# Performance work log

Hardware: AMD Instinct MI355X
Metric: run time of the kernel (lower is better)

## Reference

```python
import jax, jax.numpy as jnp
import numpy as np

B, H, W, DIM = 16, 64, 64, 512
GH, GW = 8, 8
NH = 16
HD = DIM // NH
POS = DIM // 16  # DynamicPosBias pos_dim = (dim//4)//4 = 32
EPS = 1e-5


def setup_inputs() -> dict:
    key = jax.random.key(0)
    ks = jax.random.split(key, 12)
    w = lambda k, s: jax.random.normal(k, s, jnp.float32) * 0.02
    f32 = jnp.float32
    return {
        "x": jax.random.normal(ks[0], (B, H * W, DIM), f32),
        "norm1_g": jnp.ones((DIM,), f32), "norm1_b": jnp.zeros((DIM,), f32),
        "qkv_w": w(ks[1], (3 * DIM, DIM)), "qkv_b": jnp.zeros((3 * DIM,), f32),
        "proj_w": w(ks[2], (DIM, DIM)), "proj_b": jnp.zeros((DIM,), f32),
        "pos_w0": w(ks[3], (POS, 2)), "pos_b0": jnp.zeros((POS,), f32),
        "pos_ln0_g": jnp.ones((POS,), f32), "pos_ln0_b": jnp.zeros((POS,), f32),
        "pos_w1": w(ks[4], (POS, POS)), "pos_b1": jnp.zeros((POS,), f32),
        "pos_ln1_g": jnp.ones((POS,), f32), "pos_ln1_b": jnp.zeros((POS,), f32),
        "pos_w2": w(ks[5], (POS, POS)), "pos_b2": jnp.zeros((POS,), f32),
        "pos_ln2_g": jnp.ones((POS,), f32), "pos_ln2_b": jnp.zeros((POS,), f32),
        "pos_w3": w(ks[6], (NH, POS)), "pos_b3": jnp.zeros((NH,), f32),
        "norm2_g": jnp.ones((DIM,), f32), "norm2_b": jnp.zeros((DIM,), f32),
        "mlp_w1": w(ks[7], (4 * DIM, DIM)), "mlp_b1": jnp.zeros((4 * DIM,), f32),
        "mlp_w2": w(ks[8], (DIM, 4 * DIM)), "mlp_b2": jnp.zeros((DIM,), f32),
    }


def _ln(x, g, b):
    m = jnp.mean(x, -1, keepdims=True)
    v = jnp.mean(jnp.square(x - m), -1, keepdims=True)
    return (x - m) * jax.lax.rsqrt(v + EPS) * g + b


def _rel_bias_tables():
    # relative coordinate table [(2GH-1)*(2GW-1), 2]
    ph = jnp.arange(1 - GH, GH)
    pw = jnp.arange(1 - GW, GW)
    biases = jnp.stack(jnp.meshgrid(ph, pw, indexing="ij")).reshape(2, -1).T.astype(jnp.float32)
    # relative position index [GH*GW, GH*GW]
    coords = jnp.stack(jnp.meshgrid(jnp.arange(GH), jnp.arange(GW), indexing="ij")).reshape(2, -1)
    rel = (coords[:, :, None] - coords[:, None, :]).transpose(1, 2, 0)  # [N,N,2]
    idx = (rel[..., 0] + GH - 1) * (2 * GW - 1) + (rel[..., 1] + GW - 1)
    return biases, idx


def reference(x, norm1_g, norm1_b, qkv_w, qkv_b, proj_w, proj_b,
              pos_w0, pos_b0, pos_ln0_g, pos_ln0_b,
              pos_w1, pos_b1, pos_ln1_g, pos_ln1_b,
              pos_w2, pos_b2, pos_ln2_g, pos_ln2_b,
              pos_w3, pos_b3, norm2_g, norm2_b,
              mlp_w1, mlp_b1, mlp_w2, mlp_b2):
    biases, rel_idx = _rel_bias_tables()
    Ng = GH * GW
    scale = HD ** -0.5

    shortcut = x
    h = _ln(x, norm1_g, norm1_b).reshape(B, H, W, DIM)
    # use_lda=True: long-distance (strided) grouping
    h = h.reshape(B, GH, H // GH, GW, W // GW, DIM).transpose(0, 2, 4, 1, 3, 5)
    h = h.reshape(B * (H * W) // Ng, Ng, DIM)  # [G, Ng, C]

    # attention
    qkv = h @ qkv_w.T + qkv_b
    qkv = qkv.reshape(-1, Ng, 3, NH, HD).transpose(2, 0, 3, 1, 4)  # [3,G,NH,Ng,HD]
    q, k, v = qkv[0], qkv[1], qkv[2]
    attn = jnp.einsum("ghnd,ghmd->ghnm", q * scale, k)

    # dynamic position bias MLP on the coordinate table
    p = jax.nn.relu(_ln(biases @ pos_w0.T + pos_b0, pos_ln0_g, pos_ln0_b))
    p = jax.nn.relu(_ln(p @ pos_w1.T + pos_b1, pos_ln1_g, pos_ln1_b))
    p = jax.nn.relu(_ln(p @ pos_w2.T + pos_b2, pos_ln2_g, pos_ln2_b))
    p = p @ pos_w3.T + pos_b3  # [(2GH-1)(2GW-1), NH]
    rel_bias = p[rel_idx].transpose(2, 0, 1)  # [NH, Ng, Ng]

    attn = jax.nn.softmax(attn + rel_bias[None], axis=-1)
    o = jnp.einsum("ghnm,ghmd->ghnd", attn, v)
    o = o.transpose(0, 2, 1, 3).reshape(-1, Ng, DIM)
    o = o @ proj_w.T + proj_b

    # ungroup (inverse of lda grouping)
    o = o.reshape(B, H // GH, W // GW, GH, GW, DIM)
    o = o.transpose(0, 3, 1, 4, 2, 5).reshape(B, H * W, DIM)

    x = shortcut + o
    m = _ln(x, norm2_g, norm2_b)
    m = jax.nn.gelu(m @ mlp_w1.T + mlp_b1, approximate=False)
    m = m @ mlp_w2.T + mlp_b2
    return x + m
```

## Files before the change

### kernel.cpp

```cpp
#include <hip/hip_runtime.h>
#include <hip/hip_bf16.h>

typedef __bf16 bf16;
typedef __bf16 bf16x8 __attribute__((ext_vector_type(8)));
typedef float f32x4_t __attribute__((ext_vector_type(4)));

static constexpr int kDIM = 512;

static constexpr size_t OFF_QKVW = 0;
static constexpr size_t OFF_PROJW = 1572864;
static constexpr size_t OFF_W1   = 2097152;
static constexpr size_t OFF_W2   = 4194304;
static constexpr size_t OFF_PTAB = 6291456;
static constexpr size_t OFF_A    = 8388608;
static constexpr size_t OFF_B    = 276824064;

typedef __attribute__((address_space(3))) uint32_t lds_u32_t;
typedef __attribute__((address_space(1))) const uint32_t glb_u32_t;
#define ASYNC_COPY16(gp, lp) __builtin_amdgcn_global_load_lds((glb_u32_t*)(gp), (lds_u32_t*)(lp), 16, 0, 0)
#define WAITV0() asm volatile("s_waitcnt vmcnt(0)" ::: "memory")

__global__ __launch_bounds__(256)
void cast_all_k(const float* __restrict__ qkvw, const float* __restrict__ pjw,
                const float* __restrict__ w1, const float* __restrict__ w2,
                unsigned char* __restrict__ qkvw8, unsigned char* __restrict__ pjw8,
                unsigned char* __restrict__ w18, unsigned char* __restrict__ w28)
{
    int i = blockIdx.x * blockDim.x + threadIdx.x;
    if (i < 196608) {
        float4 v = ((const float4*)qkvw)[i];
        int p = __builtin_amdgcn_cvt_pk_fp8_f32(v.x * 64.0f, v.y * 64.0f, 0, false);
        p = __builtin_amdgcn_cvt_pk_fp8_f32(v.z * 64.0f, v.w * 64.0f, p, true);
        ((unsigned int*)qkvw8)[i] = (unsigned int)p;
    } else if (i < 262144) {
        int ii = i - 196608;
        float4 v = ((const float4*)pjw)[ii];
        int idx = ii * 4;
        int row = idx >> 9;
        int j0 = idx & 511;
        float vv[4] = {v.x, v.y, v.z, v.w};
#pragma unroll
        for (int t = 0; t < 4; ++t) {
            int j = j0 + t;
            int pj = (j & ~31) | ((j & 7) << 2) | (((j >> 4) & 1) << 1) | ((j >> 3) & 1);
            int p8 = __builtin_amdgcn_cvt_pk_fp8_f32(vv[t] * 64.0f, vv[t] * 64.0f, 0, false);
            pjw8[(size_t)row * 512 + pj] = (unsigned char)(p8 & 0xff);
        }
    } else if (i < 524288) {
        int ii = i - 262144;
        float4 v = ((const float4*)w1)[ii];
        int p = __builtin_amdgcn_cvt_pk_fp8_f32(v.x * 64.0f, v.y * 64.0f, 0, false);
        p = __builtin_amdgcn_cvt_pk_fp8_f32(v.z * 64.0f, v.w * 64.0f, p, true);
        ((unsigned int*)w18)[ii] = (unsigned int)p;
    } else {
        int ii = i - 524288;
        float4 v = ((const float4*)w2)[ii];
        int idx = ii * 4;
        int row = idx >> 11;
        int j0 = idx & 2047;
        float vv[4] = {v.x, v.y, v.z, v.w};
#pragma unroll
        for (int t = 0; t < 4; ++t) {
            int j = j0 + t;
            int pj = (j & ~127) | (j & 64) | ((j & 15) << 2) | ((j >> 4) & 3);
            int p8 = __builtin_amdgcn_cvt_pk_fp8_f32(vv[t] * 64.0f, vv[t] * 64.0f, 0, false);
            w28[(size_t)row * 2048 + pj] = (unsigned char)(p8 & 0xff);
        }
    }
}

template<int GROUP>
__global__ __launch_bounds__(256)
void ln_k(const float* __restrict__ x, const float* __restrict__ gw,
          const float* __restrict__ bw, unsigned char* __restrict__ out)
{
    const int t = blockIdx.x * 4 + (threadIdx.x >> 6);
    const int lane = threadIdx.x & 63;
    const float* xp = x + (size_t)t * kDIM + lane * 8;
    float4 p0 = *(const float4*)xp;
    float4 p1 = *(const float4*)(xp + 4);
    float v[8] = {p0.x, p0.y, p0.z, p0.w, p1.x, p1.y, p1.z, p1.w};
    float s = 0.f;
#pragma unroll
    for (int i = 0; i < 8; ++i) s += v[i];
#pragma unroll
    for (int off = 32; off > 0; off >>= 1) s += __shfl_xor(s, off);
    const float mean = s * (1.0f / 512.0f);
    float q = 0.f;
#pragma unroll
    for (int i = 0; i < 8; ++i) { float d = v[i] - mean; q += d * d; }
#pragma unroll
    for (int off = 32; off > 0; off >>= 1) q += __shfl_xor(q, off);
    const float rstd = rsqrtf(q * (1.0f / 512.0f) + 1e-5f);
    size_t orow;
    if (GROUP) {
        int b = t >> 12, r = (t >> 6) & 63, c = t & 63;
        int g = b * 64 + (r & 7) * 8 + (c & 7);
        int n = (r >> 3) * 8 + (c >> 3);
        orow = (size_t)g * 64 + n;
    } else {
        orow = t;
    }
    float4 g0 = *(const float4*)(gw + lane * 8);
    float4 g1 = *(const float4*)(gw + lane * 8 + 4);
    float4 b0 = *(const float4*)(bw + lane * 8);
    float4 b1 = *(const float4*)(bw + lane * 8 + 4);
    float gg[8] = {g0.x, g0.y, g0.z, g0.w, g1.x, g1.y, g1.z, g1.w};
    float bb[8] = {b0.x, b0.y, b0.z, b0.w, b1.x, b1.y, b1.z, b1.w};
    float o[8];
#pragma unroll
    for (int i = 0; i < 8; ++i) o[i] = ((v[i] - mean) * rstd * gg[i] + bb[i]) * 32.0f;
    unsigned int lo = 0, hi = 0;
    lo = (unsigned int)__builtin_amdgcn_cvt_pk_fp8_f32(o[0], o[1], 0, false);
    lo = (unsigned int)__builtin_amdgcn_cvt_pk_fp8_f32(o[2], o[3], (int)lo, true);
    hi = (unsigned int)__builtin_amdgcn_cvt_pk_fp8_f32(o[4], o[5], 0, false);
    hi = (unsigned int)__builtin_amdgcn_cvt_pk_fp8_f32(o[6], o[7], (int)hi, true);
    uint2 u; u.x = lo; u.y = hi;
    *(uint2*)(out + orow * kDIM + lane * 8) = u;
}

__device__ inline void ln32_relu(float* h, const float* g, const float* b)
{
    float m = 0.f;
#pragma unroll
    for (int i = 0; i < 32; ++i) m += h[i];
    m *= (1.0f / 32.0f);
    float v = 0.f;
#pragma unroll
    for (int i = 0; i < 32; ++i) { float d = h[i] - m; v += d * d; }
    v *= (1.0f / 32.0f);
    float r = rsqrtf(v + 1e-5f);
#pragma unroll
    for (int i = 0; i < 32; ++i) h[i] = fmaxf((h[i] - m) * r * g[i] + b[i], 0.f);
}

__global__ __launch_bounds__(256)
void posmlp_k(const float* __restrict__ w0, const float* __restrict__ b0,
              const float* __restrict__ g0, const float* __restrict__ bb0,
              const float* __restrict__ w1, const float* __restrict__ b1,
              const float* __restrict__ g1, const float* __restrict__ bb1,
              const float* __restrict__ w2, const float* __restrict__ b2,
              const float* __restrict__ g2, const float* __restrict__ bb2,
              const float* __restrict__ w3, const float* __restrict__ b3,
              float* __restrict__ ptab)
{
    int r = threadIdx.x;
    if (r >= 225) return;
    float in0 = (float)(r / 15) - 7.0f;
    float in1 = (float)(r % 15) - 7.0f;
    float h[32], h2[32];
#pragma unroll
    for (int o = 0; o < 32; ++o) h[o] = w0[o * 2] * in0 + w0[o * 2 + 1] * in1 + b0[o];
    ln32_relu(h, g0, bb0);
#pragma unroll
    for (int o = 0; o < 32; ++o) {
        float s = b1[o];
#pragma unroll
        for (int i = 0; i < 32; ++i) s += w1[o * 32 + i] * h[i];
        h2[o] = s;
    }
    ln32_relu(h2, g1, bb1);
#pragma unroll
    for (int o = 0; o < 32; ++o) {
        float s = b2[o];
#pragma unroll
        for (int i = 0; i < 32; ++i) s += w2[o * 32 + i] * h2[i];
        h[o] = s;
    }
    ln32_relu(h, g2, bb2);
#pragma unroll
    for (int o = 0; o < 16; ++o) {
        float s = b3[o];
#pragma unroll
        for (int i = 0; i < 32; ++i) s += w3[o * 32 + i] * h[i];
        ptab[r * 16 + o] = s;
    }
}

__global__ __launch_bounds__(256)
void attn_mfma_k(const unsigned char* __restrict__ qkv, const float* __restrict__ ptab,
                 unsigned char* __restrict__ obuf)
{
    const int g  = blockIdx.x >> 1;
    const int hb = blockIdx.x & 1;
    const int w  = threadIdx.x >> 6;
    const int lane = threadIdx.x & 63;
    const int c = lane & 15, q = lane >> 4;

    __shared__ float ptl[16][240];
    __shared__ alignas(16) bf16 pl[4][4096];
    __shared__ alignas(16) bf16 vt[4][2048];

    for (int i = threadIdx.x; i < 3600; i += 256)
        ptl[i & 15][i >> 4] = ptab[i];
    __syncthreads();

    const size_t rowb = (size_t)g * 64;
    bf16* pw = pl[w];
    char* vw = (char*)vt[w];

    for (int hh = 0; hh < 2; ++hh) {
        const int head = hb * 8 + hh * 4 + w;
        const unsigned char* qb = qkv + rowb * 2048 + head * 32;

        const bf16* vbase = (const bf16*)(qb + 1024 + head * 32);
        bf16x8 vrow[4];
#pragma unroll
        for (int l = 0; l < 4; ++l)
            vrow[l] = *(const bf16x8*)((const bf16*)((const char*)vbase + (size_t)lane * 2048) + l * 8);

        long aq[4], bk[4];
#pragma unroll
        for (int i = 0; i < 4; ++i) {
            aq[i] = *(const long*)(qb + (size_t)(i * 16 + c) * 2048 + q * 8);
            bk[i] = *(const long*)(qb + 512 + (size_t)(i * 16 + c) * 2048 + q * 8);
        }

        f32x4_t s[4][4];
#pragma unroll
        for (int i = 0; i < 4; ++i)
#pragma unroll
            for (int j = 0; j < 4; ++j)
                s[i][j] = __builtin_amdgcn_mfma_f32_16x16x32_fp8_fp8(aq[i], bk[j],
                          (f32x4_t){0.f, 0.f, 0.f, 0.f}, 0, 0, 0);

#pragma unroll
        for (int l = 0; l < 4; ++l)
#pragma unroll
            for (int j = 0; j < 8; ++j) {
                const int d = l * 8 + j;
                *(bf16*)(vw + d * 128 + ((lane * 2) ^ ((d & 7) << 4))) = vrow[l][j];
            }

        const float scale = 0.17677669529663687f / 1024.0f;
        float inv[4][4];
#pragma unroll
        for (int i = 0; i < 4; ++i)
#pragma unroll
            for (int jj = 0; jj < 4; ++jj) {
                const int n = i * 16 + q * 4 + jj;
                const int na = n >> 3, nu = n & 7;
                float mx = -1e30f;
#pragma unroll
                for (int j = 0; j < 4; ++j) {
                    const int m = j * 16 + c;
                    const int idx = (na - (m >> 3) + 7) * 15 + (nu - (m & 7) + 7);
                    float v = s[i][j][jj] * scale + ptl[head][idx];
                    s[i][j][jj] = v;
                    mx = fmaxf(mx, v);
                }
#pragma unroll
                for (int off = 1; off < 16; off <<= 1) mx = fmaxf(mx, __shfl_xor(mx, off));
                float sum = 0.f;
#pragma unroll
                for (int j = 0; j < 4; ++j) {
                    float e = __expf(s[i][j][jj] - mx);
                    s[i][j][jj] = e; sum += e;
                }
#pragma unroll
                for (int off = 1; off < 16; off <<= 1) sum += __shfl_xor(sum, off);
                inv[i][jj] = __fdividef(1.0f, sum);
            }

#pragma unroll
        for (int i = 0; i < 4; ++i)
#pragma unroll
            for (int jj = 0; jj < 4; ++jj) {
                const int n = i * 16 + q * 4 + jj;
                const int swz = (n & 7) << 4;
#pragma unroll
                for (int j = 0; j < 4; ++j) {
                    const int m = j * 16 + c;
                    *(bf16*)((char*)pw + n * 128 + ((m * 2) ^ swz)) = (bf16)s[i][j][jj];
                }
            }

        bf16x8 bv[2][2];
#pragma unroll
        for (int ks = 0; ks < 2; ++ks)
#pragma unroll
            for (int dt = 0; dt < 2; ++dt)
                bv[ks][dt] = *(const bf16x8*)(vw + (dt * 16 + c) * 128 +
                              ((ks * 64 + q * 16) ^ ((c & 7) << 4)));

        f32x4_t o[4][2];
#pragma unroll
        for (int i = 0; i < 4; ++i)
#pragma unroll
            for (int dt = 0; dt < 2; ++dt)
                o[i][dt] = (f32x4_t){0.f, 0.f, 0.f, 0.f};
#pragma unroll
        for (int ks = 0; ks < 2; ++ks)
#pragma unroll
            for (int i = 0; i < 4; ++i) {
                const int n = i * 16 + c;
                bf16x8 ap = *(const bf16x8*)((char*)pw + n * 128 +
                             ((ks * 64 + q * 16) ^ ((n & 7) << 4)));
#pragma unroll
                for (int dt = 0; dt < 2; ++dt)
                    o[i][dt] = __builtin_amdgcn_mfma_f32_16x16x32_bf16(ap, bv[ks][dt], o[i][dt], 0, 0, 0);
            }

        unsigned char* ob = obuf + rowb * 512 + head * 32;
#pragma unroll
        for (int i = 0; i < 4; ++i)
#pragma unroll
            for (int jj = 0; jj < 4; ++jj) {
                const int n = i * 16 + q * 4 + jj;
                float v0 = o[i][0][jj] * inv[i][jj] * 32.0f;
                float v1 = o[i][1][jj] * inv[i][jj] * 32.0f;
                int p8 = __builtin_amdgcn_cvt_pk_fp8_f32(v0, v1, 0, false);
                *(unsigned short*)(ob + (size_t)n * 512 + c * 2) = (unsigned short)(p8 & 0xffff);
            }
    }
}

template<int MODE, int NBX, int K>
__global__ __launch_bounds__(256, 2)
void gemm_fp8(const unsigned char* __restrict__ A, const unsigned char* __restrict__ Bw,
              const float* __restrict__ bias, const float* __restrict__ resid,
              void* __restrict__ outp, int N, float invs)
{
    __shared__ alignas(16) unsigned char As[128 * 128];
    __shared__ alignas(16) unsigned char Bs[128 * 128];
    const int tid = threadIdx.x;
    const int lane = tid & 63;
    const int w = tid >> 6;
    const int wr = w >> 1, wc = w & 1;
    const int c = lane & 15, q = lane >> 4;

    const int bid = blockIdx.y * NBX + blockIdx.x;
    const int nwg = gridDim.y * NBX;
    const int swz = (bid & 7) * (nwg >> 3) + (bid >> 3);
    const int by = swz / NBX;
    const int bx = swz - by * NBX;
    const int rowBase = by * 128;
    const int colBase = bx * 128;

    f32x4_t acc[4][4];
#pragma unroll
    for (int m = 0; m < 4; ++m)
#pragma unroll
        for (int n = 0; n < 4; ++n)
            acc[m][n] = (f32x4_t){0.f, 0.f, 0.f, 0.f};

    const int key = c & 7;
    const int hb8 = (q & 1) * 8;

    const int sg = (tid & 7) ^ ((tid >> 3) & 7);
    const unsigned char* aBase = A + (size_t)(rowBase + (tid >> 3)) * K + sg * 16;
    const unsigned char* bBase = Bw + (size_t)(colBase + (tid >> 3)) * K + sg * 16;
    unsigned char* ldsA = As + (tid & 192) * 16;
    unsigned char* ldsB = Bs + (tid & 192) * 16;

#pragma unroll 2
    for (int kt = 0; kt < K; kt += 128) {
#pragma unroll
        for (int l = 0; l < 4; ++l) {
            ASYNC_COPY16(aBase + (size_t)l * 32 * K + kt, ldsA + l * 4096);
            ASYNC_COPY16(bBase + (size_t)l * 32 * K + kt, ldsB + l * 4096);
        }
        WAITV0();
        __syncthreads();
#pragma unroll
        for (int kk = 0; kk < 4; ++kk) {
            const int sb = (((2 * kk + (q >> 1)) ^ key) << 4) + hb8;
            long af[4], bfr[4];
#pragma unroll
            for (int m = 0; m < 4; ++m) {
                const int row = wr * 64 + m * 16 + c;
                af[m] = *(const long*)((const char*)As + row * 128 + sb);
            }
#pragma unroll
            for (int n = 0; n < 4; ++n) {
                const int row = wc * 64 + n * 16 + c;
                bfr[n] = *(const long*)((const char*)Bs + row * 128 + sb);
            }
#pragma unroll
            for (int m = 0; m < 4; ++m)
#pragma unroll
                for (int n = 0; n < 4; ++n)
                    acc[m][n] = __builtin_amdgcn_mfma_f32_16x16x32_fp8_fp8(af[m], bfr[n], acc[m][n], 0, 0, 0);
        }
        __syncthreads();
    }

#pragma unroll
    for (int m = 0; m < 4; ++m) {
#pragma unroll
        for (int jj = 0; jj < 4; ++jj) {
            int grow = rowBase + wr * 64 + m * 16 + q * 4 + jj;
            float vv[4];
#pragma unroll
            for (int n = 0; n < 4; ++n)
                vv[n] = acc[m][n][jj] * invs + bias[colBase + wc * 64 + n * 16 + c];
            if constexpr (MODE == 0) {
                char* ob = (char*)outp;
                if (colBase < 1024) {
                    int p0 = __builtin_amdgcn_cvt_pk_fp8_f32(vv[0] * 32.0f, vv[1] * 32.0f, 0, false);
                    int p1 = __builtin_amdgcn_cvt_pk_fp8_f32(vv[2] * 32.0f, vv[3] * 32.0f, 0, false);
                    *(unsigned short*)(ob + (size_t)grow * 2048 + colBase + wc * 64 + c * 2) =
                        (unsigned short)(p0 & 0xffff);
                    *(unsigned short*)(ob + (size_t)grow * 2048 + colBase + wc * 64 + 32 + c * 2) =
                        (unsigned short)(p1 & 0xffff);
                } else {
                    bf16 t0 = (bf16)vv[0], t1 = (bf16)vv[1], t2 = (bf16)vv[2], t3 = (bf16)vv[3];
                    unsigned int pk0 = ((unsigned int)*(unsigned short*)&t1 << 16) |
                                       (unsigned int)*(unsigned short*)&t0;
                    unsigned int pk1 = ((unsigned int)*(unsigned short*)&t3 << 16) |
                                       (unsigned int)*(unsigned short*)&t2;
                    size_t vb = (size_t)grow * 2048 + 1024 + (size_t)(colBase - 1024 + wc * 64) * 2;
                    *(unsigned int*)(ob + vb + c * 4) = pk0;
                    *(unsigned int*)(ob + vb + 64 + c * 4) = pk1;
                }
            } else if constexpr (MODE == 1) {
#pragma unroll
                for (int n = 0; n < 4; ++n) {
                    float v = vv[n];
                    float e = __expf(1.5957691216057308f * (v + 0.044715f * v * v * v));
                    vv[n] = v * __fdividef(e, 1.0f + e) * 64.0f;
                }
                int p = __builtin_amdgcn_cvt_pk_fp8_f32(vv[0], vv[1], 0, false);
                p = __builtin_amdgcn_cvt_pk_fp8_f32(vv[2], vv[3], p, true);
                *(unsigned int*)((char*)outp + (size_t)grow * N + colBase + wc * 64 + c * 4) =
                    (unsigned int)p;
            } else {
#pragma unroll
                for (int n = 0; n < 4; ++n) {
                    int gcol = colBase + wc * 64 + n * 16 + c;
                    float v = vv[n];
                    if constexpr (MODE == 2) {
                        int g = grow >> 6, ns = grow & 63;
                        int b = g >> 6, i = (g >> 3) & 7, j = g & 7;
                        int a = ns >> 3, u = ns & 7;
                        int t = b * 4096 + (a * 8 + i) * 64 + (u * 8 + j);
                        size_t oi = (size_t)t * 512 + gcol;
                        ((float*)outp)[oi] = resid[oi] + v;
                    } else {
                        size_t oi = (size_t)grow * 512 + gcol;
                        ((float*)outp)[oi] = resid[oi] + v;
                    }
                }
            }
        }
    }
}

extern "C" void kernel_launch(void* const* d_in, const int* in_sizes, int n_in,
                              void* d_out, int out_size, void* d_ws, size_t ws_size,
                              hipStream_t stream)
{
    const float* x    = (const float*)d_in[0];
    const float* n1g  = (const float*)d_in[1];
    const float* n1b  = (const float*)d_in[2];
    const float* qkvw = (const float*)d_in[3];
    const float* qkvb = (const float*)d_in[4];
    const float* pjw  = (const float*)d_in[5];
    const float* pjb  = (const float*)d_in[6];
    const float* pw0  = (const float*)d_in[7];
    const float* pb0  = (const float*)d_in[8];
    const float* pg0  = (const float*)d_in[9];
    const float* pbb0 = (const float*)d_in[10];
    const float* pw1  = (const float*)d_in[11];
    const float* pb1  = (const float*)d_in[12];
    const float* pg1  = (const float*)d_in[13];
    const float* pbb1 = (const float*)d_in[14];
    const float* pw2  = (const float*)d_in[15];
    const float* pb2  = (const float*)d_in[16];
    const float* pg2  = (const float*)d_in[17];
    const float* pbb2 = (const float*)d_in[18];
    const float* pw3  = (const float*)d_in[19];
    const float* pb3  = (const float*)d_in[20];
    const float* n2g  = (const float*)d_in[21];
    const float* n2b  = (const float*)d_in[22];
    const float* w1   = (const float*)d_in[23];
    const float* b1   = (const float*)d_in[24];
    const float* w2   = (const float*)d_in[25];
    const float* b2   = (const float*)d_in[26];

    char* ws = (char*)d_ws;
    unsigned char* qkvw_f8 = (unsigned char*)(ws + OFF_QKVW);
    unsigned char* pjw_f8  = (unsigned char*)(ws + OFF_PROJW);
    unsigned char* w1_f8 = (unsigned char*)(ws + OFF_W1);
    unsigned char* w2_f8 = (unsigned char*)(ws + OFF_W2);
    float* ptab  = (float*)(ws + OFF_PTAB);
    unsigned char* bufA8 = (unsigned char*)(ws + OFF_A);
    unsigned char* bufB8 = (unsigned char*)(ws + OFF_B);
    float* xout  = (float*)d_out;

    cast_all_k<<<3072, 256, 0, stream>>>(qkvw, pjw, w1, w2, qkvw_f8, pjw_f8, w1_f8, w2_f8);

    posmlp_k<<<1, 256, 0, stream>>>(pw0, pb0, pg0, pbb0, pw1, pb1, pg1, pbb1,
                                    pw2, pb2, pg2, pbb2, pw3, pb3, ptab);

    ln_k<1><<<16384, 256, 0, stream>>>(x, n1g, n1b, bufB8);

    gemm_fp8<0, 12, 512><<<dim3(12, 512), 256, 0, stream>>>(bufB8, qkvw_f8, qkvb, nullptr,
                                                            bufA8, 1536, 1.0f / 2048.0f);

    attn_mfma_k<<<2048, 256, 0, stream>>>(bufA8, ptab, bufB8);

    gemm_fp8<2, 4, 512><<<dim3(4, 512), 256, 0, stream>>>(bufB8, pjw_f8, pjb, x,
                                                          xout, 512, 1.0f / 2048.0f);

    ln_k<0><<<16384, 256, 0, stream>>>(xout, n2g, n2b, bufB8);

    gemm_fp8<1, 16, 512><<<dim3(16, 512), 256, 0, stream>>>(bufB8, w1_f8, b1, nullptr,
                                                            bufA8, 2048, 1.0f / 2048.0f);

    gemm_fp8<3, 4, 2048><<<dim3(4, 512), 256, 0, stream>>>(bufA8, w2_f8, b2, xout,
                                                           xout, 512, 1.0f / 4096.0f);
}
```

Before: 662.8 us.

## Use 32x32x16 FP8 MFMA GEMM kernel for MLP layers

Adds a new FP8 GEMM kernel built on 32x32x16 MFMA instructions with swizzled LDS tiles and an XOR-keyed layout, and uses it for the two MLP GEMMs. The W1 output layout (GELU epilogue writing fp8 pairs) and the W2 weight permutation are changed to match the new MFMA operand layout. The intent is higher MFMA throughput and fewer LDS reads per flop than the 16x16 variant. It risks register pressure, since launch bounds request 2 blocks per CU with four 16-wide accumulators, and it risks layout mismatches between the producer and consumer GEMMs.

```diff
diff --git a/kernel.cpp b/kernel.cpp
--- a/kernel.cpp
+++ b/kernel.cpp
@@ -4,6 +4,7 @@
 typedef __bf16 bf16;
 typedef __bf16 bf16x8 __attribute__((ext_vector_type(8)));
 typedef float f32x4_t __attribute__((ext_vector_type(4)));
+typedef float f32x16_t __attribute__((ext_vector_type(16)));
 
 static constexpr int kDIM = 512;
 
@@ -62,7 +63,7 @@
 #pragma unroll
         for (int t = 0; t < 4; ++t) {
             int j = j0 + t;
-            int pj = (j & ~127) | (j & 64) | ((j & 15) << 2) | ((j >> 4) & 3);
+            int pj = (j & ~63) | ((j & 31) << 1) | ((j >> 5) & 1);
             int p8 = __builtin_amdgcn_cvt_pk_fp8_f32(vv[t] * 64.0f, vv[t] * 64.0f, 0, false);
             w28[(size_t)row * 2048 + pj] = (unsigned char)(p8 & 0xff);
         }
@@ -413,34 +414,105 @@
                     *(unsigned int*)(ob + vb + c * 4) = pk0;
                     *(unsigned int*)(ob + vb + 64 + c * 4) = pk1;
                 }
-            } else if constexpr (MODE == 1) {
-#pragma unroll
-                for (int n = 0; n < 4; ++n) {
-                    float v = vv[n];
-                    float e = __expf(1.5957691216057308f * (v + 0.044715f * v * v * v));
-                    vv[n] = v * __fdividef(e, 1.0f + e) * 64.0f;
-                }
-                int p = __builtin_amdgcn_cvt_pk_fp8_f32(vv[0], vv[1], 0, false);
-                p = __builtin_amdgcn_cvt_pk_fp8_f32(vv[2], vv[3], p, true);
-                *(unsigned int*)((char*)outp + (size_t)grow * N + colBase + wc * 64 + c * 4) =
-                    (unsigned int)p;
             } else {
 #pragma unroll
                 for (int n = 0; n < 4; ++n) {
                     int gcol = colBase + wc * 64 + n * 16 + c;
                     float v = vv[n];
-                    if constexpr (MODE == 2) {
-                        int g = grow >> 6, ns = grow & 63;
-                        int b = g >> 6, i = (g >> 3) & 7, j = g & 7;
-                        int a = ns >> 3, u = ns & 7;
-                        int t = b * 4096 + (a * 8 + i) * 64 + (u * 8 + j);
-                        size_t oi = (size_t)t * 512 + gcol;
-                        ((float*)outp)[oi] = resid[oi] + v;
-                    } else {
-                        size_t oi = (size_t)grow * 512 + gcol;
-                        ((float*)outp)[oi] = resid[oi] + v;
-                    }
+                    int g = grow >> 6, ns = grow & 63;
+                    int b = g >> 6, i = (g >> 3) & 7, j = g & 7;
+                    int a = ns >> 3, u = ns & 7;
+                    int t = b * 4096 + (a * 8 + i) * 64 + (u * 8 + j);
+                    size_t oi = (size_t)t * 512 + gcol;
+                    ((float*)outp)[oi] = resid[oi] + v;
                 }
+            }
+        }
+    }
+}
+
+template<int MODE, int NBX, int K>
+__global__ __launch_bounds__(256, 2)
+void gemm_fp8_32(const unsigned char* __restrict__ A, const unsigned char* __restrict__ Bw,
+                 const float* __restrict__ bias, const float* __restrict__ resid,
+                 void* __restrict__ outp, int N, float invs)
+{
+    __shared__ alignas(16) unsigned char As[128 * 128];
+    __shared__ alignas(16) unsigned char Bs[128 * 128];
+    const int tid = threadIdx.x;
+    const int lane = tid & 63;
+    const int w = tid >> 6;
+    const int wr = w >> 1, wc = w & 1;
+    const int c32 = lane & 31, hb = lane >> 5;
+
+    const int bid = blockIdx.y * NBX + blockIdx.x;
+    const int nwg = gridDim.y * NBX;
+    const int swz = (bid & 7) * (nwg >> 3) + (bid >> 3);
+    const int by = swz / NBX;
+    const int bx = swz - by * NBX;
+    const int rowBase = by * 128;
+    const int colBase = bx * 128;
+
+    f32x16_t acc00 = {0.f,0.f,0.f,0.f,0.f,0.f,0.f,0.f,0.f,0.f,0.f,0.f,0.f,0.f,0.f,0.f};
+    f32x16_t acc01 = acc00, acc10 = acc00, acc11 = acc00;
+
+    const int key = c32 & 7;
+    const int hb8 = hb * 8;
+    const int rA0 = (wr * 64 + c32) * 128;
+    const int rB0 = (wc * 64 + c32) * 128;
+
+    const int sg = (tid & 7) ^ ((tid >> 3) & 7);
+    const unsigned char* aBase = A + (size_t)(rowBase + (tid >> 3)) * K + sg * 16;
+    const unsigned char* bBase = Bw + (size_t)(colBase + (tid >> 3)) * K + sg * 16;
+    unsigned char* ldsA = As + (tid & 192) * 16;
+    unsigned char* ldsB = Bs + (tid & 192) * 16;
+
+#pragma unroll 2
+    for (int kt = 0; kt < K; kt += 128) {
+#pragma unroll
+        for (int l = 0; l < 4; ++l) {
+            ASYNC_COPY16(aBase + (size_t)l * 32 * K + kt, ldsA + l * 4096);
+            ASYNC_COPY16(bBase + (size_t)l * 32 * K + kt, ldsB + l * 4096);
+        }
+        WAITV0();
+        __syncthreads();
+#pragma unroll
+        for (int ks = 0; ks < 8; ++ks) {
+            const int so = ((ks ^ key) << 4) + hb8;
+            long a0 = *(const long*)((const char*)As + rA0 + so);
+            long a1 = *(const long*)((const char*)As + rA0 + 32 * 128 + so);
+            long b0 = *(const long*)((const char*)Bs + rB0 + so);
+            long b1 = *(const long*)((const char*)Bs + rB0 + 32 * 128 + so);
+            acc00 = __builtin_amdgcn_mfma_f32_32x32x16_fp8_fp8(a0, b0, acc00, 0, 0, 0);
+            acc01 = __builtin_amdgcn_mfma_f32_32x32x16_fp8_fp8(a0, b1, acc01, 0, 0, 0);
+            acc10 = __builtin_amdgcn_mfma_f32_32x32x16_fp8_fp8(a1, b0, acc10, 0, 0, 0);
+            acc11 = __builtin_amdgcn_mfma_f32_32x32x16_fp8_fp8(a1, b1, acc11, 0, 0, 0);
+        }
+        __syncthreads();
+    }
+
+    const float bs0 = bias[colBase + wc * 64 + c32];
+    const float bs1 = bias[colBase + wc * 64 + 32 + c32];
+#pragma unroll
+    for (int mt = 0; mt < 2; ++mt) {
+#pragma unroll
+        for (int r = 0; r < 16; ++r) {
+            const int grow = rowBase + wr * 64 + mt * 32 + (r & 3) + ((r >> 2) << 3) + hb * 4;
+            float v0 = (mt == 0 ? acc00[r] : acc10[r]) * invs + bs0;
+            float v1 = (mt == 0 ? acc01[r] : acc11[r]) * invs + bs1;
+            if constexpr (MODE == 1) {
+                float e0 = __expf(1.5957691216057308f * (v0 + 0.044715f * v0 * v0 * v0));
+                v0 = v0 * __fdividef(e0, 1.0f + e0) * 64.0f;
+                float e1 = __expf(1.5957691216057308f * (v1 + 0.044715f * v1 * v1 * v1));
+                v1 = v1 * __fdividef(e1, 1.0f + e1) * 64.0f;
+                int p = __builtin_amdgcn_cvt_pk_fp8_f32(v0, v1, 0, false);
+                *(unsigned short*)((char*)outp + (size_t)grow * N + colBase + wc * 64 + c32 * 2) =
+                    (unsigned short)(p & 0xffff);
+            } else {
+                size_t o0 = (size_t)grow * 512 + colBase + wc * 64 + c32;
+                size_t o1 = o0 + 32;
+                ((float*)outp)[o0] = resid[o0] + v0;
+                ((float*)outp)[o1] = resid[o1] + v1;
             }
         }
     }
@@ -505,9 +577,9 @@
 
     ln_k<0><<<16384, 256, 0, stream>>>(xout, n2g, n2b, bufB8);
 
-    gemm_fp8<1, 16, 512><<<dim3(16, 512), 256, 0, stream>>>(bufB8, w1_f8, b1, nullptr,
-                                                            bufA8, 2048, 1.0f / 2048.0f);
-
-    gemm_fp8<3, 4, 2048><<<dim3(4, 512), 256, 0, stream>>>(bufA8, w2_f8, b2, xout,
-                                                           xout, 512, 1.0f / 4096.0f);
-}
+    gemm_fp8_32<1, 16, 512><<<dim3(16, 512), 256, 0, stream>>>(bufB8, w1_f8, b1, nullptr,
+                                                               bufA8, 2048, 1.0f / 2048.0f);
+
+    gemm_fp8_32<3, 4, 2048><<<dim3(4, 512), 256, 0, stream>>>(bufA8, w2_f8, b2, xout,
+                                                              xout, 512, 1.0f / 4096.0f);
+}
```

After: 687.4 us. 3.7% more time.
